# Kernel optimization log

Hardware: AMD Instinct MI355X
Metric: run time of the kernel (lower is better)

The kernel has to match this reference:

```python
import jax, jax.numpy as jnp
import numpy as np

N_NODES = 50000
N_EDGES = 800000
C = 4      # num_channels
F_IN = 64
F_OUT = 64


def setup_inputs() -> dict:
    key = jax.random.key(0)
    k0, k1, k2, k3 = jax.random.split(key, 4)
    x = jax.random.normal(k0, (N_NODES, C, F_IN), dtype=jnp.float32)
    edge_index = jax.random.randint(k1, (2, N_EDGES), 0, N_NODES, dtype=jnp.int64)
    edge_weight = jax.random.uniform(k2, (N_EDGES,), dtype=jnp.float32)
    # per-channel GCNConv weights (glorot-ish) and biases
    W = jax.random.normal(k3, (C, F_IN, F_OUT), dtype=jnp.float32) / jnp.sqrt(jnp.float32(F_IN))
    b = jnp.zeros((C, F_OUT), dtype=jnp.float32)
    return {"x": x, "edge_index": edge_index, "edge_weight": edge_weight, "W": W, "b": b}


def reference(x, edge_index, edge_weight, W, b):
    # Batched-over-channels GCNConv (normalize=True, add_self_loops=True):
    # out[:, c, :] = D^{-1/2} (A + I) D^{-1/2} (x[:, c, :] @ W[c]) + b[c]
    n = x.shape[0]
    loop = jnp.arange(n, dtype=edge_index.dtype)
    row = jnp.concatenate([edge_index[0], loop])   # source
    col = jnp.concatenate([edge_index[1], loop])   # target
    ew = jnp.concatenate([edge_weight, jnp.ones((n,), dtype=edge_weight.dtype)])
    deg = jax.ops.segment_sum(ew, col, num_segments=n)
    dinv = jnp.where(deg > 0, jax.lax.rsqrt(deg), jnp.zeros_like(deg))
    norm = dinv[row] * ew * dinv[col]              # [E+N]
    xw = jnp.einsum('ncf,cfo->nco', x, W)          # per-channel linear transform
    msgs = xw[row] * norm[:, None, None]           # gather + scale, [E+N, C, F_OUT]
    out = jax.ops.segment_sum(msgs, col, num_segments=n)  # scatter-add
    return out + b[None, :, :]
```

## Files before the change

kernel.cpp:

```cpp
#include <hip/hip_runtime.h>

#define C_CH 4
#define F_INN 64
#define F_OUTT 64
#define CF 256
#define FIXP 33554432.0f
#define XSP 68
#define MAXDEG 72

static __device__ __forceinline__ unsigned rne16(float f) {
    unsigned u = __float_as_uint(f);
    return (u + 0x7fffu + ((u >> 16) & 1u)) >> 16;
}
static __device__ __forceinline__ unsigned pk2(float a, float b) {
    return rne16(a) | (rne16(b) << 16);
}

__global__ __launch_bounds__(256) void histxw_kernel(
        const int* __restrict__ row, const int* __restrict__ col,
        const float* __restrict__ ew,
        unsigned long long* __restrict__ cd64, unsigned* __restrict__ edata4, int E,
        const float* __restrict__ x, const float* __restrict__ W,
        unsigned* __restrict__ xwb, int n) {
    __shared__ float xs[64][XSP];
    __shared__ float ws[64][64];
    int t = threadIdx.x;
    int bid = blockIdx.x;

    int e = bid * 256 + t;
    bool has = (e < E);
    unsigned long long old = 0;
    int esrc = 0, edst = 0;
    float w = 0.f;
    if (has) {
        edst = col[e];
        esrc = row[e];
        w = ew[e];
        unsigned fx = __float2uint_rn(w * FIXP);
        old = atomicAdd(&cd64[edst], (1ULL << 32) | (unsigned long long)fx);
    }

    int c = bid & 3;
    int N0 = (bid >> 2) * 64;
    {
        const float4* Wc4 = reinterpret_cast<const float4*>(W + (size_t)c * F_INN * F_OUTT);
        float4* ws4 = reinterpret_cast<float4*>(&ws[0][0]);
#pragma unroll
        for (int r = 0; r < 4; ++r) ws4[t + 256 * r] = Wc4[t + 256 * r];
    }
    {
        int r = t >> 2;
        int node = N0 + r;
        int kq = (t & 3) * 4;
        const float* __restrict__ xrow = x + (size_t)node * CF + c * F_INN;
#pragma unroll
        for (int rep = 0; rep < 4; ++rep) {
            int k = kq + rep * 16;
            float4 v = (node < n) ? *reinterpret_cast<const float4*>(xrow + k)
                                  : make_float4(0.f, 0.f, 0.f, 0.f);
            xs[k + 0][r] = v.x;
            xs[k + 1][r] = v.y;
            xs[k + 2][r] = v.z;
            xs[k + 3][r] = v.w;
        }
    }
    __syncthreads();

    int fi = t & 15;
    int ni = t >> 4;
    float acc[4][4];
#pragma unroll
    for (int j = 0; j < 4; ++j)
#pragma unroll
        for (int o = 0; o < 4; ++o) acc[j][o] = 0.f;

#pragma unroll 8
    for (int k = 0; k < F_INN; ++k) {
        float4 a = *reinterpret_cast<const float4*>(&xs[k][4 * ni]);
        float4 b = *reinterpret_cast<const float4*>(&ws[k][4 * fi]);
        float av[4] = {a.x, a.y, a.z, a.w};
        float bv[4] = {b.x, b.y, b.z, b.w};
#pragma unroll
        for (int j = 0; j < 4; ++j)
#pragma unroll
            for (int o = 0; o < 4; ++o) acc[j][o] = fmaf(av[j], bv[o], acc[j][o]);
    }

#pragma unroll
    for (int j = 0; j < 4; ++j) {
        int node = N0 + 4 * ni + j;
        if (node < n) {
            uint2 pkd;
            pkd.x = pk2(acc[j][0], acc[j][1]);
            pkd.y = pk2(acc[j][2], acc[j][3]);
            size_t eidx = (size_t)node * CF + c * F_OUTT + 4 * fi;
            *reinterpret_cast<uint2*>(xwb + (eidx >> 1)) = pkd;
        }
    }

    if (has) {
        unsigned rk = (unsigned)(old >> 32);
        if (rk < MAXDEG)
            edata4[(size_t)edst * MAXDEG + rk] = (unsigned)esrc | (rne16(w) << 16);
    }
}

__global__ __launch_bounds__(256) void fixup_kernel(
        const unsigned long long* __restrict__ cd64,
        unsigned* __restrict__ edata4, float* __restrict__ dinv, int n) {
    int v = (int)((blockIdx.x * 256u + threadIdx.x) >> 6);
    int lane = threadIdx.x & 63;
    if (v >= n) return;
    unsigned long long cd = cd64[v];
    int cnt = (int)(cd >> 32);
    if (cnt > MAXDEG) cnt = MAXDEG;
    float dv = rsqrtf(1.0f + (float)(unsigned)(cd & 0xffffffffULL) * (1.0f / FIXP));
    if (lane == 0) dinv[v] = dv;
    unsigned* __restrict__ bp = edata4 + (size_t)v * MAXDEG;
    for (int j = lane; j < cnt; j += 64) {
        unsigned e = bp[j];
        int src = (int)(e & 0xffffu);
        unsigned long long cs = cd64[src];
        float ds = rsqrtf(1.0f + (float)(unsigned)(cs & 0xffffffffULL) * (1.0f / FIXP));
        float w = __uint_as_float(e & 0xffff0000u) * ds;
        bp[j] = (e & 0xffffu) | (rne16(w) << 16);
    }
}

__global__ __launch_bounds__(256) void gather_kernel(const unsigned long long* __restrict__ cd64,
                                                     const unsigned* __restrict__ edata4,
                                                     const float* __restrict__ dinv,
                                                     const unsigned* __restrict__ xwb,
                                                     const float* __restrict__ b,
                                                     float* __restrict__ out, int n) {
    int v = (int)((blockIdx.x * 256u + threadIdx.x) >> 6);
    int lane = threadIdx.x & 63;
    if (v >= n) return;

    int cnt = (int)(cd64[v] >> 32);
    if (cnt > MAXDEG) cnt = MAXDEG;
    const unsigned* __restrict__ ept = edata4 + (size_t)v * MAXDEG;
    float di = dinv[v];

    const uint2* __restrict__ xw2 = reinterpret_cast<const uint2*>(xwb);
    uint2 uself = xw2[(size_t)v * 64 + lane];
    const float4 bv = *reinterpret_cast<const float4*>(b + lane * 4);
    float4 acc;
    acc.x = __uint_as_float(uself.x << 16) * di;
    acc.y = __uint_as_float(uself.x & 0xffff0000u) * di;
    acc.z = __uint_as_float(uself.y << 16) * di;
    acc.w = __uint_as_float(uself.y & 0xffff0000u) * di;

    int j = 0;
    int e8 = cnt & ~7;
    for (; j < e8; j += 8) {
        unsigned ee[8];
        uint2 uu[8];
#pragma unroll
        for (int q = 0; q < 8; ++q) ee[q] = ept[j + q];
#pragma unroll
        for (int q = 0; q < 8; ++q) uu[q] = xw2[(size_t)(ee[q] & 0xffffu) * 64 + lane];
#pragma unroll
        for (int q = 0; q < 8; ++q) {
            float nn = __uint_as_float(ee[q] & 0xffff0000u);
            acc.x = fmaf(__uint_as_float(uu[q].x << 16), nn, acc.x);
            acc.y = fmaf(__uint_as_float(uu[q].x & 0xffff0000u), nn, acc.y);
            acc.z = fmaf(__uint_as_float(uu[q].y << 16), nn, acc.z);
            acc.w = fmaf(__uint_as_float(uu[q].y & 0xffff0000u), nn, acc.w);
        }
    }
    int e4 = j + ((cnt - j) & ~3);
    for (; j < e4; j += 4) {
        unsigned ee[4];
        uint2 uu[4];
#pragma unroll
        for (int q = 0; q < 4; ++q) ee[q] = ept[j + q];
#pragma unroll
        for (int q = 0; q < 4; ++q) uu[q] = xw2[(size_t)(ee[q] & 0xffffu) * 64 + lane];
#pragma unroll
        for (int q = 0; q < 4; ++q) {
            float nn = __uint_as_float(ee[q] & 0xffff0000u);
            acc.x = fmaf(__uint_as_float(uu[q].x << 16), nn, acc.x);
            acc.y = fmaf(__uint_as_float(uu[q].x & 0xffff0000u), nn, acc.y);
            acc.z = fmaf(__uint_as_float(uu[q].y << 16), nn, acc.z);
            acc.w = fmaf(__uint_as_float(uu[q].y & 0xffff0000u), nn, acc.w);
        }
    }
    for (; j < cnt; ++j) {
        unsigned e = ept[j];
        float nn = __uint_as_float(e & 0xffff0000u);
        uint2 u0 = xw2[(size_t)(e & 0xffffu) * 64 + lane];
        acc.x = fmaf(__uint_as_float(u0.x << 16), nn, acc.x);
        acc.y = fmaf(__uint_as_float(u0.x & 0xffff0000u), nn, acc.y);
        acc.z = fmaf(__uint_as_float(u0.y << 16), nn, acc.z);
        acc.w = fmaf(__uint_as_float(u0.y & 0xffff0000u), nn, acc.w);
    }
    float4 o;
    o.x = fmaf(acc.x, di, bv.x);
    o.y = fmaf(acc.y, di, bv.y);
    o.z = fmaf(acc.z, di, bv.z);
    o.w = fmaf(acc.w, di, bv.w);
    *reinterpret_cast<float4*>(out + (size_t)v * CF + lane * 4) = o;
}

extern "C" void kernel_launch(void* const* d_in, const int* in_sizes, int n_in,
                              void* d_out, int out_size, void* d_ws, size_t ws_size,
                              hipStream_t stream) {
    const float* x  = (const float*)d_in[0];
    const int*   ei = (const int*)d_in[1];
    const float* ew = (const float*)d_in[2];
    const float* W  = (const float*)d_in[3];
    const float* b  = (const float*)d_in[4];
    float* out = (float*)d_out;

    int n = in_sizes[0] / (C_CH * F_INN);
    int E = in_sizes[2];

    const int* row = ei;
    const int* col = ei + E;

    auto align_up = [](size_t v) { return (v + 255) & ~(size_t)255; };
    char* p = (char*)d_ws;
    unsigned long long* cd64 = (unsigned long long*)p;  p += align_up((size_t)n * 8);
    float* dinv = (float*)p;                 p += align_up((size_t)n * 4);
    unsigned* edata4 = (unsigned*)p;         p += align_up((size_t)n * MAXDEG * 4);
    unsigned* xwb = (unsigned*)p;

    int nbFused = ((n + 63) / 64) * C_CH;

    (void)hipMemsetAsync(cd64, 0, (size_t)n * 8, stream);
    histxw_kernel<<<nbFused, 256, 0, stream>>>(row, col, ew, cd64, edata4, E, x, W, xwb, n);
    fixup_kernel<<<(n * 64 + 255) / 256, 256, 0, stream>>>(cd64, edata4, dinv, n);
    gather_kernel<<<(n * 64 + 255) / 256, 256, 0, stream>>>(cd64, edata4, dinv, xwb, b, out, n);
}
```

Before: 136.9 us.

## Fuse degree-normalization fixup into gather via wave-wide edge load and shuffles

Removes the separate fixup kernel. The gather kernel now loads each node's edge list once across lanes, computes source dinv there, and broadcasts source index and weight with __shfl. This drops one launch, the read-modify-write of edata4 and the dinv buffer, and replaces per-lane redundant edge loads with shuffles. It also changes the LDS padding of the xs tile from 68 to 64, which may add bank conflicts on the transposed stores.

```diff
diff --git a/kernel.cpp b/kernel.cpp
--- a/kernel.cpp
+++ b/kernel.cpp
@@ -5,7 +5,7 @@
 #define F_OUTT 64
 #define CF 256
 #define FIXP 33554432.0f
-#define XSP 68
+#define XSP 64
 #define MAXDEG 72
 
 static __device__ __forceinline__ unsigned rne16(float f) {
@@ -14,6 +14,9 @@
 }
 static __device__ __forceinline__ unsigned pk2(float a, float b) {
     return rne16(a) | (rne16(b) << 16);
+}
+static __device__ __forceinline__ float unpack_dinv(unsigned long long cd) {
+    return rsqrtf(1.0f + (float)(unsigned)(cd & 0xffffffffULL) * (1.0f / FIXP));
 }
 
 __global__ __launch_bounds__(256) void histxw_kernel(
@@ -105,31 +108,8 @@
     }
 }
 
-__global__ __launch_bounds__(256) void fixup_kernel(
-        const unsigned long long* __restrict__ cd64,
-        unsigned* __restrict__ edata4, float* __restrict__ dinv, int n) {
-    int v = (int)((blockIdx.x * 256u + threadIdx.x) >> 6);
-    int lane = threadIdx.x & 63;
-    if (v >= n) return;
-    unsigned long long cd = cd64[v];
-    int cnt = (int)(cd >> 32);
-    if (cnt > MAXDEG) cnt = MAXDEG;
-    float dv = rsqrtf(1.0f + (float)(unsigned)(cd & 0xffffffffULL) * (1.0f / FIXP));
-    if (lane == 0) dinv[v] = dv;
-    unsigned* __restrict__ bp = edata4 + (size_t)v * MAXDEG;
-    for (int j = lane; j < cnt; j += 64) {
-        unsigned e = bp[j];
-        int src = (int)(e & 0xffffu);
-        unsigned long long cs = cd64[src];
-        float ds = rsqrtf(1.0f + (float)(unsigned)(cs & 0xffffffffULL) * (1.0f / FIXP));
-        float w = __uint_as_float(e & 0xffff0000u) * ds;
-        bp[j] = (e & 0xffffu) | (rne16(w) << 16);
-    }
-}
-
 __global__ __launch_bounds__(256) void gather_kernel(const unsigned long long* __restrict__ cd64,
                                                      const unsigned* __restrict__ edata4,
-                                                     const float* __restrict__ dinv,
                                                      const unsigned* __restrict__ xwb,
                                                      const float* __restrict__ b,
                                                      float* __restrict__ out, int n) {
@@ -137,10 +117,20 @@
     int lane = threadIdx.x & 63;
     if (v >= n) return;
 
-    int cnt = (int)(cd64[v] >> 32);
+    unsigned long long cd = cd64[v];
+    int cnt = (int)(cd >> 32);
     if (cnt > MAXDEG) cnt = MAXDEG;
+    float di = unpack_dinv(cd);
     const unsigned* __restrict__ ept = edata4 + (size_t)v * MAXDEG;
-    float di = dinv[v];
+
+    unsigned eA = (lane < cnt) ? ept[lane] : 0u;
+    unsigned eB = (lane + 64 < cnt) ? ept[lane + 64] : 0u;
+    int srcA = (int)(eA & 0xffffu), srcB = (int)(eB & 0xffffu);
+    float wA = 0.f, wB = 0.f;
+    if (lane < cnt)
+        wA = __uint_as_float(eA & 0xffff0000u) * unpack_dinv(cd64[srcA]);
+    if (lane + 64 < cnt)
+        wB = __uint_as_float(eB & 0xffff0000u) * unpack_dinv(cd64[srcB]);
 
     const uint2* __restrict__ xw2 = reinterpret_cast<const uint2*>(xwb);
     uint2 uself = xw2[(size_t)v * 64 + lane];
@@ -151,50 +141,67 @@
     acc.z = __uint_as_float(uself.y << 16) * di;
     acc.w = __uint_as_float(uself.y & 0xffff0000u) * di;
 
+    int c1 = (cnt < 64) ? cnt : 64;
     int j = 0;
-    int e8 = cnt & ~7;
+    int e8 = c1 & ~7;
     for (; j < e8; j += 8) {
-        unsigned ee[8];
+        float nn[8];
+        int ss[8];
         uint2 uu[8];
 #pragma unroll
-        for (int q = 0; q < 8; ++q) ee[q] = ept[j + q];
-#pragma unroll
-        for (int q = 0; q < 8; ++q) uu[q] = xw2[(size_t)(ee[q] & 0xffffu) * 64 + lane];
-#pragma unroll
         for (int q = 0; q < 8; ++q) {
-            float nn = __uint_as_float(ee[q] & 0xffff0000u);
-            acc.x = fmaf(__uint_as_float(uu[q].x << 16), nn, acc.x);
-            acc.y = fmaf(__uint_as_float(uu[q].x & 0xffff0000u), nn, acc.y);
-            acc.z = fmaf(__uint_as_float(uu[q].y << 16), nn, acc.z);
-            acc.w = fmaf(__uint_as_float(uu[q].y & 0xffff0000u), nn, acc.w);
-        }
-    }
-    int e4 = j + ((cnt - j) & ~3);
+            nn[q] = __shfl(wA, j + q);
+            ss[q] = __shfl(srcA, j + q);
+        }
+#pragma unroll
+        for (int q = 0; q < 8; ++q) uu[q] = xw2[(size_t)ss[q] * 64 + lane];
+#pragma unroll
+        for (int q = 0; q < 8; ++q) {
+            acc.x = fmaf(__uint_as_float(uu[q].x << 16), nn[q], acc.x);
+            acc.y = fmaf(__uint_as_float(uu[q].x & 0xffff0000u), nn[q], acc.y);
+            acc.z = fmaf(__uint_as_float(uu[q].y << 16), nn[q], acc.z);
+            acc.w = fmaf(__uint_as_float(uu[q].y & 0xffff0000u), nn[q], acc.w);
+        }
+    }
+    int e4 = j + ((c1 - j) & ~3);
     for (; j < e4; j += 4) {
-        unsigned ee[4];
+        float nn[4];
+        int ss[4];
         uint2 uu[4];
 #pragma unroll
-        for (int q = 0; q < 4; ++q) ee[q] = ept[j + q];
-#pragma unroll
-        for (int q = 0; q < 4; ++q) uu[q] = xw2[(size_t)(ee[q] & 0xffffu) * 64 + lane];
-#pragma unroll
         for (int q = 0; q < 4; ++q) {
-            float nn = __uint_as_float(ee[q] & 0xffff0000u);
-            acc.x = fmaf(__uint_as_float(uu[q].x << 16), nn, acc.x);
-            acc.y = fmaf(__uint_as_float(uu[q].x & 0xffff0000u), nn, acc.y);
-            acc.z = fmaf(__uint_as_float(uu[q].y << 16), nn, acc.z);
-            acc.w = fmaf(__uint_as_float(uu[q].y & 0xffff0000u), nn, acc.w);
-        }
-    }
-    for (; j < cnt; ++j) {
-        unsigned e = ept[j];
-        float nn = __uint_as_float(e & 0xffff0000u);
-        uint2 u0 = xw2[(size_t)(e & 0xffffu) * 64 + lane];
+            nn[q] = __shfl(wA, j + q);
+            ss[q] = __shfl(srcA, j + q);
+        }
+#pragma unroll
+        for (int q = 0; q < 4; ++q) uu[q] = xw2[(size_t)ss[q] * 64 + lane];
+#pragma unroll
+        for (int q = 0; q < 4; ++q) {
+            acc.x = fmaf(__uint_as_float(uu[q].x << 16), nn[q], acc.x);
+            acc.y = fmaf(__uint_as_float(uu[q].x & 0xffff0000u), nn[q], acc.y);
+            acc.z = fmaf(__uint_as_float(uu[q].y << 16), nn[q], acc.z);
+            acc.w = fmaf(__uint_as_float(uu[q].y & 0xffff0000u), nn[q], acc.w);
+        }
+    }
+    for (; j < c1; ++j) {
+        float nn = __shfl(wA, j);
+        int ss = __shfl(srcA, j);
+        uint2 u0 = xw2[(size_t)ss * 64 + lane];
         acc.x = fmaf(__uint_as_float(u0.x << 16), nn, acc.x);
         acc.y = fmaf(__uint_as_float(u0.x & 0xffff0000u), nn, acc.y);
         acc.z = fmaf(__uint_as_float(u0.y << 16), nn, acc.z);
         acc.w = fmaf(__uint_as_float(u0.y & 0xffff0000u), nn, acc.w);
     }
+    for (j = 64; j < cnt; ++j) {
+        float nn = __shfl(wB, j - 64);
+        int ss = __shfl(srcB, j - 64);
+        uint2 u0 = xw2[(size_t)ss * 64 + lane];
+        acc.x = fmaf(__uint_as_float(u0.x << 16), nn, acc.x);
+        acc.y = fmaf(__uint_as_float(u0.x & 0xffff0000u), nn, acc.y);
+        acc.z = fmaf(__uint_as_float(u0.y << 16), nn, acc.z);
+        acc.w = fmaf(__uint_as_float(u0.y & 0xffff0000u), nn, acc.w);
+    }
+
     float4 o;
     o.x = fmaf(acc.x, di, bv.x);
     o.y = fmaf(acc.y, di, bv.y);
@@ -222,7 +229,6 @@
     auto align_up = [](size_t v) { return (v + 255) & ~(size_t)255; };
     char* p = (char*)d_ws;
     unsigned long long* cd64 = (unsigned long long*)p;  p += align_up((size_t)n * 8);
-    float* dinv = (float*)p;                 p += align_up((size_t)n * 4);
     unsigned* edata4 = (unsigned*)p;         p += align_up((size_t)n * MAXDEG * 4);
     unsigned* xwb = (unsigned*)p;
 
@@ -230,6 +236,5 @@
 
     (void)hipMemsetAsync(cd64, 0, (size_t)n * 8, stream);
     histxw_kernel<<<nbFused, 256, 0, stream>>>(row, col, ew, cd64, edata4, E, x, W, xwb, n);
-    fixup_kernel<<<(n * 64 + 255) / 256, 256, 0, stream>>>(cd64, edata4, dinv, n);
-    gather_kernel<<<(n * 64 + 255) / 256, 256, 0, stream>>>(cd64, edata4, dinv, xwb, b, out, n);
-}
+    gather_kernel<<<(n * 64 + 255) / 256, 256, 0, stream>>>(cd64, edata4, xwb, b, out, n);
+}
```

Result: faster. 126.6 us (-7.5%).
